# Performance work log

Hardware: AMD Instinct MI355X
Metric: run time of the kernel (lower is better)

Reference implementation:

```python
import jax, jax.numpy as jnp
import numpy as np
import math

F, M, C, OUT = 60, 600, 8, 18  # feature_size, max_samples, cluster_size, output_dim
B = 2048


def l2_normalize(x, axis):
    # matches tf.nn.l2_normalize (epsilon=1e-12)
    sq = jnp.sum(jnp.square(x), axis=axis, keepdims=True)
    return x * jax.lax.rsqrt(jnp.maximum(sq, 1e-12))


def setup_inputs() -> dict:
    key = jax.random.key(0)
    k = jax.random.split(key, 6)
    s1 = 1.0 / math.sqrt(F)
    s2 = 1.0 / math.sqrt(C)
    return {
        "reshaped_input": jax.random.normal(k[0], (B * M, F), dtype=jnp.float32),
        "cluster_weights": jax.random.normal(k[1], (F, C), dtype=jnp.float32) * s1,
        "covar_weights": jax.random.normal(k[2], (F, C), dtype=jnp.float32) * s1,
        "cluster_biases": jax.random.normal(k[3], (C,), dtype=jnp.float32) * s1,
        "cluster_weights2": jax.random.normal(k[4], (1, F, C), dtype=jnp.float32) * s1,
        "hidden1_weights": jax.random.normal(k[5], (2 * C * F, OUT), dtype=jnp.float32) * s2,
    }


def reference(reshaped_input, cluster_weights, covar_weights, cluster_biases,
              cluster_weights2, hidden1_weights):
    cw = jnp.square(covar_weights) + 1e-6                      # [F, C]

    act = reshaped_input @ cluster_weights + cluster_biases    # [B*M, C]
    act = jax.nn.softmax(act, axis=-1)
    act = act.reshape(-1, M, C)                                # [B, M, C]

    a_sum = jnp.sum(act, axis=-2, keepdims=True)               # [B, 1, C]
    a = a_sum * cluster_weights2                               # [B, F, C]

    x = reshaped_input.reshape(-1, M, F)                       # [B, M, F]

    fv1 = jnp.einsum('bmc,bmf->bfc', act, x)                   # [B, F, C]
    fv2 = jnp.einsum('bmc,bmf->bfc', act, jnp.square(x))       # [B, F, C]

    a2 = a_sum * jnp.square(cluster_weights2)                  # [B, F, C]
    b2 = fv1 * cluster_weights2                                # [B, F, C]

    fv2 = a2 + fv2 - 2.0 * b2
    fv2 = fv2 / jnp.square(cw)
    fv2 = fv2 - a_sum                                          # broadcast [B,1,C]
    fv2 = fv2.reshape(-1, C * F)
    fv2 = l2_normalize(fv2, axis=1)
    fv2 = l2_normalize(fv2, axis=1)  # second normalize as in original (idempotent)

    fv1 = (fv1 - a) / cw                                       # [B, F, C]
    fv1 = l2_normalize(fv1, axis=1)                            # per-cluster, along F
    fv1 = fv1.reshape(-1, C * F)
    fv1 = l2_normalize(fv1, axis=1)

    fv = jnp.concatenate([fv1, fv2], axis=1)                   # [B, 2*C*F]
    return fv @ hidden1_weights                                # [B, OUT]
```

## Files before the change

kernel.cpp:

```cpp
#include <hip/hip_runtime.h>
#include <hip/hip_bf16.h>

#define FDIM 60
#define MROW 600
#define CDIM 8
#define ODIM 18
#define CH   120
#define NCHUNK 5
#define BLK  512

typedef short bf16x8 __attribute__((ext_vector_type(8)));
typedef float f32x4  __attribute__((ext_vector_type(4)));

__device__ __forceinline__ unsigned int pk2(float lo, float hi) {
    __hip_bfloat162 h2 = __float22bfloat162_rn(make_float2(lo, hi));
    unsigned int u;
    __builtin_memcpy(&u, &h2, sizeof(u));
    return u;
}
__device__ __forceinline__ short f2bf(float f) {
    __hip_bfloat16 h = __float2bfloat16(f);
    short s;
    __builtin_memcpy(&s, &h, sizeof(s));
    return s;
}

#define WAVE_LGKM() do {                                          \
    asm volatile("s_waitcnt lgkmcnt(0)" ::: "memory");            \
    __builtin_amdgcn_sched_barrier(0);                            \
} while (0)
#define RAW_BAR() do {                                            \
    asm volatile("s_waitcnt lgkmcnt(0)" ::: "memory");            \
    __builtin_amdgcn_s_barrier();                                 \
    __builtin_amdgcn_sched_barrier(0);                            \
} while (0)

__global__ void __launch_bounds__(BLK, 4) netfv_kernel(
    const float* __restrict__ x,
    const float* __restrict__ W,
    const float* __restrict__ covar,
    const float* __restrict__ bias,
    const float* __restrict__ cw2,
    const float* __restrict__ H,
    float* __restrict__ out)
{
    __shared__ __align__(16) short xsT1[64 * 136];
    __shared__ __align__(16) short xsT2[64 * 136];
    __shared__ __align__(16) short xsM [128 * 88];
    __shared__ __align__(16) short actT[16 * 136];
    __shared__ __align__(16) short WtB [16 * 72];
    __shared__ __align__(16) float fvbuf[1024];
    __shared__ __align__(16) float fvl[960];
    __shared__ float redA[64], redB[64];
    __shared__ float asuml[8], n1rs[8], n1c_s[8], n2c_s[8], scal[2];

    const int tid  = threadIdx.x;
    const int b    = blockIdx.x;
    const int lane = tid & 63;
    const int wv   = tid >> 6;
    const int mg   = tid >> 3;
    const int fs   = tid & 7;
    const int ln15 = lane & 15;
    const int quad = lane >> 4;
    const int fvsel = wv & 1;
    const int tile  = wv >> 1;

    const size_t rowbase = (size_t)b * (MROW * FDIM);
    const bool stv = (mg < 60);
    const float* prow = x + rowbase + (size_t)(2 * mg) * FDIM + 8 * fs;
    const int mloc = wv * 16 + ln15;
    const bool vm = (mloc < CH);

    float4 A0, A1, B0, B1;
    A0 = A1 = B0 = B1 = make_float4(0.f, 0.f, 0.f, 0.f);
    if (stv) {
        A0 = *(const float4*)prow;
        A1 = *(const float4*)(prow + FDIM);
        if (fs < 7) { B0 = *(const float4*)(prow + 4); B1 = *(const float4*)(prow + FDIM + 4); }
    }

    {
        int c = tid >> 5, j = tid & 31;
        float v0 = (2 * j     < FDIM) ? W[(2 * j) * CDIM + (c & 7)]     : 0.f;
        float v1 = (2 * j + 1 < FDIM) ? W[(2 * j + 1) * CDIM + (c & 7)] : 0.f;
        if (c >= CDIM) { v0 = 0.f; v1 = 0.f; }
        ((unsigned int*)WtB)[c * 36 + j] = pk2(v0, v1);
    }
    {
        unsigned int* z1 = (unsigned int*)xsT1;
        unsigned int* z2 = (unsigned int*)xsT2;
        for (int i = tid; i < 64 * 68; i += BLK) { z1[i] = 0u; z2[i] = 0u; }
        unsigned int* zm = (unsigned int*)(xsM + 120 * 88);
        for (int i = tid; i < 8 * 44; i += BLK) zm[i] = 0u;
        unsigned int* az = (unsigned int*)(actT + 8 * 136);
        for (int i = tid; i < 544; i += BLK) az[i] = 0u;
    }
    __syncthreads();

    const bf16x8 aw0 = *(const bf16x8*)(WtB + ln15 * 72 + quad * 8);
    const bf16x8 aw1 = *(const bf16x8*)(WtB + ln15 * 72 + 32 + quad * 8);
    const float4 lb  = *(const float4*)(bias + (quad & 1) * 4);

    f32x4 acc = {0.f, 0.f, 0.f, 0.f};
    float asum_acc[4] = {0.f, 0.f, 0.f, 0.f};

    for (int ck = 0; ck < NCHUNK; ++ck) {
        float4 nA0, nA1, nB0, nB1;
        nA0 = nA1 = nB0 = nB1 = make_float4(0.f, 0.f, 0.f, 0.f);
        if (ck + 1 < NCHUNK && stv) {
            const float* pn = prow + (size_t)(ck + 1) * (CH * FDIM);
            nA0 = *(const float4*)pn;
            nA1 = *(const float4*)(pn + FDIM);
            if (fs < 7) { nB0 = *(const float4*)(pn + 4); nB1 = *(const float4*)(pn + FDIM + 4); }
        }

        if (stv) {
            float xv0[8] = {A0.x, A0.y, A0.z, A0.w, B0.x, B0.y, B0.z, B0.w};
            float xv1[8] = {A1.x, A1.y, A1.z, A1.w, B1.x, B1.y, B1.z, B1.w};
            {
                unsigned int q0 = pk2(xv0[0], xv0[1]), q1 = pk2(xv0[2], xv0[3]);
                unsigned int q2 = pk2(xv0[4], xv0[5]), q3 = pk2(xv0[6], xv0[7]);
                *(uint4*)(xsM + (2 * mg) * 88 + 8 * fs) = make_uint4(q0, q1, q2, q3);
                unsigned int s0 = pk2(xv1[0], xv1[1]), s1 = pk2(xv1[2], xv1[3]);
                unsigned int s2 = pk2(xv1[4], xv1[5]), s3 = pk2(xv1[6], xv1[7]);
                *(uint4*)(xsM + (2 * mg + 1) * 88 + 8 * fs) = make_uint4(s0, s1, s2, s3);
            }
            const int wbase = (((mg >> 2) ^ fs) << 2) + (mg & 3);
            #pragma unroll
            for (int i = 0; i < 8; ++i) {
                int woff = (8 * fs + i) * 68 + wbase;
                ((unsigned int*)xsT1)[woff] = pk2(xv0[i], xv1[i]);
                ((unsigned int*)xsT2)[woff] = pk2(xv0[i] * xv0[i], xv1[i] * xv1[i]);
            }
        }

        WAVE_LGKM();
        {
            bf16x8 bv0 = *(const bf16x8*)(xsM + mloc * 88 + quad * 8);
            bf16x8 bv1 = *(const bf16x8*)(xsM + mloc * 88 + 32 + quad * 8);
            f32x4 lz = {0.f, 0.f, 0.f, 0.f};
            lz = __builtin_amdgcn_mfma_f32_16x16x32_bf16(aw0, bv0, lz, 0, 0, 0);
            lz = __builtin_amdgcn_mfma_f32_16x16x32_bf16(aw1, bv1, lz, 0, 0, 0);
            float L0 = lz[0] + lb.x, L1 = lz[1] + lb.y;
            float L2 = lz[2] + lb.z, L3 = lz[3] + lb.w;
            float mx = fmaxf(fmaxf(L0, L1), fmaxf(L2, L3));
            mx = fmaxf(mx, __shfl_xor(mx, 16));
            float e0 = __expf(L0 - mx), e1 = __expf(L1 - mx);
            float e2 = __expf(L2 - mx), e3 = __expf(L3 - mx);
            float s = e0 + e1 + e2 + e3;
            s += __shfl_xor(s, 16);
            float inv = __builtin_amdgcn_rcpf(s);
            if (quad < 2) {
                float a0  = vm ? e0 * inv : 0.f, a1v = vm ? e1 * inv : 0.f;
                float a2v = vm ? e2 * inv : 0.f, a3v = vm ? e3 * inv : 0.f;
                asum_acc[0] += a0;  asum_acc[1] += a1v;
                asum_acc[2] += a2v; asum_acc[3] += a3v;
                actT[(quad * 4 + 0) * 136 + mloc] = f2bf(a0);
                actT[(quad * 4 + 1) * 136 + mloc] = f2bf(a1v);
                actT[(quad * 4 + 2) * 136 + mloc] = f2bf(a2v);
                actT[(quad * 4 + 3) * 136 + mloc] = f2bf(a3v);
            }
        }
        RAW_BAR();

        {
            const short* xsel = fvsel ? xsT2 : xsT1;
            const int f   = tile * 16 + ln15;
            const int fsw = f >> 3;
            #pragma unroll
            for (int ks = 0; ks < 4; ++ks) {
                bf16x8 av = *(const bf16x8*)(actT + ln15 * 136 + ks * 32 + quad * 8);
                int kblk = ks * 4 + quad;
                bf16x8 bv = *(const bf16x8*)(xsel + f * 136 + ((kblk ^ fsw) << 3));
                acc = __builtin_amdgcn_mfma_f32_16x16x32_bf16(av, bv, acc, 0, 0, 0);
            }
        }
        RAW_BAR();

        A0 = nA0; A1 = nA1; B0 = nB0; B1 = nB1;
    }

    #pragma unroll
    for (int r = 0; r < 4; ++r) {
        float v = asum_acc[r];
        v += __shfl_xor(v, 1); v += __shfl_xor(v, 2);
        v += __shfl_xor(v, 4); v += __shfl_xor(v, 8);
        asum_acc[r] = v;
    }
    if (quad < 2 && ln15 == 0) {
        #pragma unroll
        for (int r = 0; r < 4; ++r) redA[wv * 8 + quad * 4 + r] = asum_acc[r];
    }
    __syncthreads();
    if (tid < 64) {
        float v = redA[tid];
        v += __shfl_down(v, 8); v += __shfl_down(v, 16); v += __shfl_down(v, 32);
        if (tid < 8) asuml[tid] = v;
    }
    if (quad < 2) {
        #pragma unroll
        for (int r = 0; r < 4; ++r)
            fvbuf[fvsel * 512 + (tile * 16 + ln15) * 8 + quad * 4 + r] = acc[r];
    }
    __syncthreads();

    float fv1v = 0.f, fv2v = 0.f;
    const int f_e = tid >> 3, c_e = tid & 7;
    if (tid < 480) {
        float fv1r = fvbuf[f_e * 8 + c_e];
        float fv2r = fvbuf[512 + f_e * 8 + c_e];
        float asv  = asuml[c_e];
        float cw2v = cw2[f_e * 8 + c_e];
        float cv   = covar[f_e * 8 + c_e];
        float cwv  = cv * cv + 1e-6f;
        float rcw  = 1.0f / cwv;
        fv1v = (fv1r - asv * cw2v) * rcw;
        fv2v = (fmaf(asv * cw2v, cw2v, fv2r) - 2.0f * fv1r * cw2v) * rcw * rcw - asv;
    }

    {
        float p1 = fv1v * fv1v, p2 = fv2v * fv2v;
        p1 += __shfl_down(p1, 8);  p2 += __shfl_down(p2, 8);
        p1 += __shfl_down(p1, 16); p2 += __shfl_down(p2, 16);
        p1 += __shfl_down(p1, 32); p2 += __shfl_down(p2, 32);
        if (lane < 8) { redA[wv * 8 + lane] = p1; redB[wv * 8 + lane] = p2; }
    }
    __syncthreads();
    if (tid < 64) {
        float q1 = redA[tid], q2 = redB[tid];
        q1 += __shfl_down(q1, 8);  q2 += __shfl_down(q2, 8);
        q1 += __shfl_down(q1, 16); q2 += __shfl_down(q2, 16);
        q1 += __shfl_down(q1, 32); q2 += __shfl_down(q2, 32);
        if (tid < 8) { n1c_s[tid] = q1; n2c_s[tid] = q2; }
    }
    __syncthreads();
    if (tid == 0) {
        float S1 = 0.f, S2 = 0.f;
        #pragma unroll
        for (int c = 0; c < 8; ++c) {
            float rs = rsqrtf(fmaxf(n1c_s[c], 1e-12f));
            n1rs[c] = rs;
            S1 += n1c_s[c] * rs * rs;
            S2 += n2c_s[c];
        }
        scal[0] = rsqrtf(fmaxf(S1, 1e-12f));
        scal[1] = rsqrtf(fmaxf(S2, 1e-12f));
    }
    __syncthreads();
    if (tid < 480) {
        fvl[f_e * 8 + c_e]       = fv1v * n1rs[c_e] * scal[0];
        fvl[480 + f_e * 8 + c_e] = fv2v * scal[1];
    }
    __syncthreads();

    for (int o = wv; o < ODIM; o += 8) {
        float sacc = 0.f;
        #pragma unroll 5
        for (int i = lane; i < 960; i += 64)
            sacc = fmaf(fvl[i], H[i * ODIM + o], sacc);
        sacc += __shfl_down(sacc, 32);
        sacc += __shfl_down(sacc, 16);
        sacc += __shfl_down(sacc, 8);
        sacc += __shfl_down(sacc, 4);
        sacc += __shfl_down(sacc, 2);
        sacc += __shfl_down(sacc, 1);
        if (lane == 0) out[(size_t)b * ODIM + o] = sacc;
    }
}

extern "C" void kernel_launch(void* const* d_in, const int* in_sizes, int n_in,
                              void* d_out, int out_size, void* d_ws, size_t ws_size,
                              hipStream_t stream) {
    const float* x     = (const float*)d_in[0];
    const float* W     = (const float*)d_in[1];
    const float* covar = (const float*)d_in[2];
    const float* bias  = (const float*)d_in[3];
    const float* cw2   = (const float*)d_in[4];
    const float* H     = (const float*)d_in[5];
    float* outp = (float*)d_out;

    const int Bn = in_sizes[0] / (MROW * FDIM);
    hipLaunchKernelGGL(netfv_kernel, dim3(Bn), dim3(BLK), 0, stream,
                       x, W, covar, bias, cw2, H, outp);
}
```

Baseline: 432.3 us.

## Drop squared-x LDS buffer, square on the fly, alias shared buffers for occupancy

Removes the separate xsT2 buffer holding bf16 x^2. Half the waves now square the bf16 x values after loading them from xsT1, which also changes the rounding of x^2. The xsM padding is shrunk, epilogue scratch arrays are aliased onto the xsT1 and actT buffers, and launch bounds are raised to 6 blocks per CU so that more blocks can be resident. LDS staging is moved ahead of the next-chunk global prefetch, and this adds conversion ALU work in the MFMA loop.

```diff
diff --git a/kernel.cpp b/kernel.cpp
--- a/kernel.cpp
+++ b/kernel.cpp
@@ -35,7 +35,7 @@
     __builtin_amdgcn_sched_barrier(0);                            \
 } while (0)
 
-__global__ void __launch_bounds__(BLK, 4) netfv_kernel(
+__global__ void __launch_bounds__(BLK, 6) netfv_kernel(
     const float* __restrict__ x,
     const float* __restrict__ W,
     const float* __restrict__ covar,
@@ -45,14 +45,19 @@
     float* __restrict__ out)
 {
     __shared__ __align__(16) short xsT1[64 * 136];
-    __shared__ __align__(16) short xsT2[64 * 136];
-    __shared__ __align__(16) short xsM [128 * 88];
+    __shared__ __align__(16) short xsM [120 * 72];
     __shared__ __align__(16) short actT[16 * 136];
     __shared__ __align__(16) short WtB [16 * 72];
-    __shared__ __align__(16) float fvbuf[1024];
-    __shared__ __align__(16) float fvl[960];
-    __shared__ float redA[64], redB[64];
-    __shared__ float asuml[8], n1rs[8], n1c_s[8], n2c_s[8], scal[2];
+
+    float* const fvbuf = (float*)xsT1;
+    float* const fvl   = (float*)xsT1 + 1024;
+    float* const redA  = (float*)actT;
+    float* const redB  = redA + 64;
+    float* const asuml = redB + 64;
+    float* const n1rs  = asuml + 8;
+    float* const n1c_s = n1rs + 8;
+    float* const n2c_s = n1c_s + 8;
+    float* const scal  = n2c_s + 8;
 
     const int tid  = threadIdx.x;
     const int b    = blockIdx.x;
@@ -70,6 +75,7 @@
     const float* prow = x + rowbase + (size_t)(2 * mg) * FDIM + 8 * fs;
     const int mloc = wv * 16 + ln15;
     const bool vm = (mloc < CH);
+    const int mrow = vm ? mloc : 0;
 
     float4 A0, A1, B0, B1;
     A0 = A1 = B0 = B1 = make_float4(0.f, 0.f, 0.f, 0.f);
@@ -88,10 +94,7 @@
     }
     {
         unsigned int* z1 = (unsigned int*)xsT1;
-        unsigned int* z2 = (unsigned int*)xsT2;
-        for (int i = tid; i < 64 * 68; i += BLK) { z1[i] = 0u; z2[i] = 0u; }
-        unsigned int* zm = (unsigned int*)(xsM + 120 * 88);
-        for (int i = tid; i < 8 * 44; i += BLK) zm[i] = 0u;
+        for (int i = tid; i < 64 * 68; i += BLK) z1[i] = 0u;
         unsigned int* az = (unsigned int*)(actT + 8 * 136);
         for (int i = tid; i < 544; i += BLK) az[i] = 0u;
     }
@@ -105,6 +108,26 @@
     float asum_acc[4] = {0.f, 0.f, 0.f, 0.f};
 
     for (int ck = 0; ck < NCHUNK; ++ck) {
+        if (stv) {
+            float xv0[8] = {A0.x, A0.y, A0.z, A0.w, B0.x, B0.y, B0.z, B0.w};
+            float xv1[8] = {A1.x, A1.y, A1.z, A1.w, B1.x, B1.y, B1.z, B1.w};
+            {
+                unsigned int q0 = pk2(xv0[0], xv0[1]), q1 = pk2(xv0[2], xv0[3]);
+                unsigned int q2 = pk2(xv0[4], xv0[5]), q3 = pk2(xv0[6], xv0[7]);
+                *(uint4*)(xsM + (2 * mg) * 72 + 8 * fs) = make_uint4(q0, q1, q2, q3);
+                unsigned int s0 = pk2(xv1[0], xv1[1]), s1 = pk2(xv1[2], xv1[3]);
+                unsigned int s2 = pk2(xv1[4], xv1[5]), s3 = pk2(xv1[6], xv1[7]);
+                *(uint4*)(xsM + (2 * mg + 1) * 72 + 8 * fs) = make_uint4(s0, s1, s2, s3);
+            }
+            const int wbase = (((mg >> 2) ^ fs) << 2) + (mg & 3);
+            #pragma unroll
+            for (int i = 0; i < 8; ++i) {
+                int woff = (8 * fs + i) * 68 + wbase;
+                ((unsigned int*)xsT1)[woff] = pk2(xv0[i], xv1[i]);
+            }
+        }
+        __builtin_amdgcn_sched_barrier(0);
+
         float4 nA0, nA1, nB0, nB1;
         nA0 = nA1 = nB0 = nB1 = make_float4(0.f, 0.f, 0.f, 0.f);
         if (ck + 1 < NCHUNK && stv) {
@@ -114,30 +137,10 @@
             if (fs < 7) { nB0 = *(const float4*)(pn + 4); nB1 = *(const float4*)(pn + FDIM + 4); }
         }
 
-        if (stv) {
-            float xv0[8] = {A0.x, A0.y, A0.z, A0.w, B0.x, B0.y, B0.z, B0.w};
-            float xv1[8] = {A1.x, A1.y, A1.z, A1.w, B1.x, B1.y, B1.z, B1.w};
-            {
-                unsigned int q0 = pk2(xv0[0], xv0[1]), q1 = pk2(xv0[2], xv0[3]);
-                unsigned int q2 = pk2(xv0[4], xv0[5]), q3 = pk2(xv0[6], xv0[7]);
-                *(uint4*)(xsM + (2 * mg) * 88 + 8 * fs) = make_uint4(q0, q1, q2, q3);
-                unsigned int s0 = pk2(xv1[0], xv1[1]), s1 = pk2(xv1[2], xv1[3]);
-                unsigned int s2 = pk2(xv1[4], xv1[5]), s3 = pk2(xv1[6], xv1[7]);
-                *(uint4*)(xsM + (2 * mg + 1) * 88 + 8 * fs) = make_uint4(s0, s1, s2, s3);
-            }
-            const int wbase = (((mg >> 2) ^ fs) << 2) + (mg & 3);
-            #pragma unroll
-            for (int i = 0; i < 8; ++i) {
-                int woff = (8 * fs + i) * 68 + wbase;
-                ((unsigned int*)xsT1)[woff] = pk2(xv0[i], xv1[i]);
-                ((unsigned int*)xsT2)[woff] = pk2(xv0[i] * xv0[i], xv1[i] * xv1[i]);
-            }
-        }
-
         WAVE_LGKM();
         {
-            bf16x8 bv0 = *(const bf16x8*)(xsM + mloc * 88 + quad * 8);
-            bf16x8 bv1 = *(const bf16x8*)(xsM + mloc * 88 + 32 + quad * 8);
+            bf16x8 bv0 = *(const bf16x8*)(xsM + mrow * 72 + quad * 8);
+            bf16x8 bv1 = *(const bf16x8*)(xsM + mrow * 72 + 32 + quad * 8);
             f32x4 lz = {0.f, 0.f, 0.f, 0.f};
             lz = __builtin_amdgcn_mfma_f32_16x16x32_bf16(aw0, bv0, lz, 0, 0, 0);
             lz = __builtin_amdgcn_mfma_f32_16x16x32_bf16(aw1, bv1, lz, 0, 0, 0);
@@ -164,14 +167,24 @@
         RAW_BAR();
 
         {
-            const short* xsel = fvsel ? xsT2 : xsT1;
             const int f   = tile * 16 + ln15;
             const int fsw = f >> 3;
             #pragma unroll
             for (int ks = 0; ks < 4; ++ks) {
                 bf16x8 av = *(const bf16x8*)(actT + ln15 * 136 + ks * 32 + quad * 8);
                 int kblk = ks * 4 + quad;
-                bf16x8 bv = *(const bf16x8*)(xsel + f * 136 + ((kblk ^ fsw) << 3));
+                bf16x8 bv = *(const bf16x8*)(xsT1 + f * 136 + ((kblk ^ fsw) << 3));
+                if (fvsel) {
+                    union { bf16x8 v; unsigned short us[8]; unsigned int u[4]; } in, sq;
+                    in.v = bv;
+                    #pragma unroll
+                    for (int p = 0; p < 4; ++p) {
+                        float lo = __uint_as_float((unsigned)in.us[2 * p]     << 16);
+                        float hi = __uint_as_float((unsigned)in.us[2 * p + 1] << 16);
+                        sq.u[p] = pk2(lo * lo, hi * hi);
+                    }
+                    bv = sq.v;
+                }
                 acc = __builtin_amdgcn_mfma_f32_16x16x32_bf16(av, bv, acc, 0, 0, 0);
             }
         }
```

Result: no change. 430.9 us (-0.3%).
